# Kernel optimization log

Hardware: AMD Instinct MI355X
Metric: run time of the kernel (lower is better)

The kernel has to match this reference:

```python
import jax, jax.numpy as jnp
import numpy as np

SR = 44100.0
BLK = 512          # block_size (hop)
WL = 2048          # win_length
W4 = WL // 4
B, NF = 4, 512
L = NF * BLK


def _framewise_conv(src, kernels, pad_l, pad_r):
    """Per-(batch,frame) 1D cross-correlation via grouped conv.
    src: (B,F,blk), kernels: (B,F,kw) -> (B,F,blk+pad_l+pad_r-kw+1)."""
    b, f, blk = src.shape
    kw = kernels.shape[-1]
    s = jnp.pad(src, ((0, 0), (0, 0), (pad_l, pad_r))).reshape(1, b * f, blk + pad_l + pad_r)
    k = kernels.reshape(b * f, 1, kw)
    out = jax.lax.conv_general_dilated(
        s, k, window_strides=(1,), padding='VALID',
        feature_group_count=b * f, dimension_numbers=('NCH', 'OIH', 'NCH'))
    return out.reshape(b, f, -1)


def _overlap_add(frames, hop, out_len):
    """frames: (B,F,FL) -> (B,out_len) overlap-add with stride hop (== F.fold)."""
    b, f, fl = frames.shape
    idx = jnp.arange(f)[:, None] * hop + jnp.arange(fl)[None, :]  # (F,FL)
    out = jnp.zeros((b, out_len), frames.dtype)
    return out.at[:, idx].add(frames)


def setup_inputs() -> dict:
    key = jax.random.key(0)
    k1, k2, k3, k4, k5 = jax.random.split(key, 5)
    f0_frames = jax.random.uniform(k1, (B, NF, 1), jnp.float32) * 320.0 + 80.0  # 80-400 Hz
    hk = jax.random.normal(k2, (B, NF, WL), jnp.float32) * (1.0 / np.sqrt(WL))
    hks = jax.random.normal(k3, (B, NF, W4), jnp.float32) * (1.0 / np.sqrt(W4))
    nk = jax.random.normal(k4, (B, NF, W4), jnp.float32) * (1.0 / np.sqrt(W4))
    static_noise = jax.random.uniform(k5, (WL * 127,), jnp.float32) * 2.0 - 1.0
    return {"f0_frames": f0_frames, "harmonic_filt_kernel": hk,
            "harmonic_filt_kernel_short": hks, "noise_filt_kernel": nk,
            "static_noise": static_noise}


def reference(f0_frames, harmonic_filt_kernel, harmonic_filt_kernel_short,
              noise_filt_kernel, static_noise):
    b, nf, _ = f0_frames.shape
    # f0 upsampled to sample rate: (B, L)
    f0 = jnp.repeat(f0_frames, BLK, axis=2).reshape(b, -1)
    # phase accumulator, fractional part (f0 > 0 so frac == mod 1)
    x = jnp.mod(jnp.cumsum(f0 / SR, axis=1), 1.0)
    pix = jnp.pi * x
    a = jnp.round(SR / jnp.clip(f0, 20.0, None) * 0.5) * 2.0 + 1.0
    # band-limited impulse-train-like harmonic source (Dirichlet kernel)
    harmonic_source = jnp.where(pix < 1e-8, 1.0,
                                jnp.sin(a * pix) / (a * jnp.sin(pix)))
    harmonic_source = harmonic_source.reshape(b, nf, BLK)
    # tiled static noise, same for all batch items
    reps = L // static_noise.shape[0] + 1
    noise = jnp.tile(static_noise * 0.3162, reps)[:L].reshape(1, nf, BLK)
    noise = jnp.broadcast_to(noise, (b, nf, BLK))
    # short per-frame FIR on harmonic source and noise (kernel len WL//4)
    hs_short = _framewise_conv(harmonic_source, harmonic_filt_kernel_short, W4, W4 - 1)
    nz = _framewise_conv(noise, noise_filt_kernel, W4, W4 - 1)
    # overlap-add mix, crop to L samples
    mix = _overlap_add(nz + hs_short, BLK, L + W4)[:, :L]
    # long per-frame FIR (kernel len WL) on the mixed signal
    src2 = mix.reshape(b, nf, BLK)
    h2 = _framewise_conv(src2, harmonic_filt_kernel, WL, WL - 1)
    out = _overlap_add(h2, BLK, L + WL)[:, :L]
    return jnp.clip(out, -1.0, 1.0)
```

## Files before the change

### kernel.cpp

```cpp
#include <hip/hip_runtime.h>


#define BLKS  512
#define WL    2048
#define W4    512
#define NB    4
#define NFR   512
#define LTOT  (NFR*BLKS)
#define NCH   (LTOT/16)
#define SN_LEN 260096

typedef float f4 __attribute__((ext_vector_type(4)));

static __device__ __forceinline__ void step16(const f4 hA, const f4 hB, const f4 x,
                                              float& a0, float& a1, float& a2, float& a3) {
    a0 += hB.x*x.x; a0 += hB.y*x.y; a0 += hB.z*x.z; a0 += hB.w*x.w;
    a1 += hA.w*x.x; a1 += hB.x*x.y; a1 += hB.y*x.z; a1 += hB.z*x.w;
    a2 += hA.z*x.x; a2 += hA.w*x.y; a2 += hB.x*x.z; a2 += hB.y*x.w;
    a3 += hA.y*x.x; a3 += hA.z*x.y; a3 += hA.w*x.z; a3 += hB.x*x.w;
}

static __device__ __forceinline__ void seg4(const float* __restrict__ P, int c0,
                                            const float* __restrict__ S,
                                            float& a0, float& a1, float& a2, float& a3) {
    f4 hA = *(const f4*)(P + c0 - 4);
    #pragma unroll 4
    for (int m0 = 0; m0 < 512; m0 += 4) {
        f4 hB = *(const f4*)(P + c0 + m0);
        f4 x  = *(const f4*)(S + m0);
        step16(hA, hB, x, a0, a1, a2, a3);
        hA = hB;
    }
}

static __device__ __forceinline__ void seg4x2(const float* __restrict__ Ph,
                                              const float* __restrict__ Pn, int c0,
                                              const float* __restrict__ Sh,
                                              const float* __restrict__ Sn,
                                              float& a0, float& a1, float& a2, float& a3) {
    f4 hA = *(const f4*)(Ph + c0 - 4);
    f4 nA = *(const f4*)(Pn + c0 - 4);
    #pragma unroll 2
    for (int m0 = 0; m0 < 512; m0 += 4) {
        f4 hB = *(const f4*)(Ph + c0 + m0);
        f4 nB = *(const f4*)(Pn + c0 + m0);
        f4 xh = *(const f4*)(Sh + m0);
        f4 xn = *(const f4*)(Sn + m0);
        a0 += hB.x*xh.x + nB.x*xn.x;  a0 += hB.y*xh.y + nB.y*xn.y;
        a0 += hB.z*xh.z + nB.z*xn.z;  a0 += hB.w*xh.w + nB.w*xn.w;
        a1 += hA.w*xh.x + nA.w*xn.x;  a1 += hB.x*xh.y + nB.x*xn.y;
        a1 += hB.y*xh.z + nB.y*xn.z;  a1 += hB.z*xh.w + nB.z*xn.w;
        a2 += hA.z*xh.x + nA.z*xn.x;  a2 += hA.w*xh.y + nA.w*xn.y;
        a2 += hB.x*xh.z + nB.x*xn.z;  a2 += hB.y*xh.w + nB.y*xn.w;
        a3 += hA.y*xh.x + nA.y*xn.x;  a3 += hA.z*xh.y + nA.z*xn.y;
        a3 += hA.w*xh.z + nA.w*xn.z;  a3 += hB.x*xh.w + nB.x*xn.w;
        hA = hB; nA = nB;
    }
}

__global__ void __launch_bounds__(256) k_scan_a(const float* __restrict__ f0_frames,
                                                float* __restrict__ L0,
                                                float* __restrict__ L1) {
    int b = blockIdx.y;
    int chunk = blockIdx.x * 256 + threadIdx.x;
    int g0 = chunk * 16;
    float d = f0_frames[b*NFR + (g0 >> 9)] / 44100.0f;
    float* o = L0 + (size_t)b*LTOT + g0;
    float acc = 0.0f;
    #pragma unroll
    for (int j = 0; j < 16; ++j) { acc = acc + d; o[j] = acc; }
    L1[(size_t)b*NCH + chunk] = acc;
}

__global__ void __launch_bounds__(1024) k_scan_b(float* __restrict__ L1g) {
    __shared__ float sL2[1024];
    __shared__ float sL3[64];
    __shared__ float sL4[4];
    int b = blockIdx.x, tid = threadIdx.x;
    float* L1 = L1g + (size_t)b*NCH;
    {
        float* p = L1 + tid*16;
        float acc = 0.0f;
        #pragma unroll
        for (int j = 0; j < 16; ++j) { acc = acc + p[j]; p[j] = acc; }
        sL2[tid] = acc;
    }
    __syncthreads();
    if (tid < 64) {
        float acc = 0.0f;
        #pragma unroll
        for (int j = 0; j < 16; ++j) { acc = acc + sL2[tid*16+j]; sL2[tid*16+j] = acc; }
        sL3[tid] = acc;
    }
    __syncthreads();
    if (tid < 4) {
        float acc = 0.0f;
        #pragma unroll
        for (int j = 0; j < 16; ++j) { acc = acc + sL3[tid*16+j]; sL3[tid*16+j] = acc; }
        sL4[tid] = acc;
    }
    __syncthreads();
    if (tid == 0) {
        float acc = 0.0f;
        #pragma unroll
        for (int j = 0; j < 4; ++j) { acc = acc + sL4[j]; sL4[j] = acc; }
    }
    __syncthreads();
    if (tid >= 16 && tid < 64) sL3[tid] = sL3[tid] + sL4[tid/16 - 1];
    __syncthreads();
    if (tid >= 16) sL2[tid] = sL2[tid] + sL3[tid/16 - 1];
    __syncthreads();
    for (int i = tid; i < NCH; i += 1024)
        if (i >= 16) L1[i] = L1[i] + sL2[i/16 - 1];
}

__global__ void __launch_bounds__(256) k_source(const float* __restrict__ f0_frames,
                                                const float* __restrict__ L0,
                                                const float* __restrict__ L1,
                                                float* __restrict__ hs) {
    int F = blockIdx.x, b = blockIdx.y;
    int tid = threadIdx.x;
    float f0 = f0_frames[b*NFR + F];
    float af = rintf(44100.0f / fmaxf(f0, 20.0f) * 0.5f) * 2.0f + 1.0f;
    const float PIF = 3.14159274101257324f;
    for (int i = tid; i < BLKS; i += 256) {
        int g = F*BLKS + i;
        float c = L0[(size_t)b*LTOT + g];
        if (g >= 16) c = c + L1[(size_t)b*NCH + (g >> 4) - 1];
        float x = c - floorf(c);
        float pix = PIF * x;
        float v;
        if (pix < 1e-8f) v = 1.0f;
        else             v = sinf(af * pix) / (af * sinf(pix));
        hs[(size_t)b*LTOT + g] = v;
    }
}

__global__ void __launch_bounds__(128) k_mix(const float* __restrict__ hs,
                                             const float* __restrict__ sn,
                                             const float* __restrict__ hks,
                                             const float* __restrict__ nk,
                                             float* __restrict__ mixg) {
    __shared__ float sH[1024], sN[1024];
    __shared__ float Hh1[1024], Hn1[1024];
    __shared__ float Hh0[1024], Hn0[1024];
    int F = blockIdx.x, b = blockIdx.y, tid = threadIdx.x;
    int s0 = (F - 1) * BLKS;
    for (int i = tid; i < 1024; i += 128) {
        int s = s0 + i;
        float hv = 0.0f, nv = 0.0f;
        if (s >= 0) { hv = hs[(size_t)b*LTOT + s]; nv = sn[s % SN_LEN] * 0.3162f; }
        sH[i] = hv; sN[i] = nv;
    }
    const float* kh = hks + ((size_t)b*NFR + F)*W4;
    const float* kn = nk  + ((size_t)b*NFR + F)*W4;
    for (int i = tid; i < 1024; i += 128) {
        Hh1[i] = (i < 512) ? kh[i] : 0.0f;
        Hn1[i] = (i < 512) ? kn[i] : 0.0f;
        float hp = 0.0f, np_ = 0.0f;
        if (i >= 512 && F >= 1) { hp = kh[i - 1024]; np_ = kn[i - 1024]; }
        Hh0[i] = hp; Hn0[i] = np_;
    }
    __syncthreads();
    int j0 = tid * 4;
    float a0=0.f, a1=0.f, a2=0.f, a3=0.f;
    seg4x2(Hh1, Hn1, 512 - j0, sH + 512, sN + 512, a0, a1, a2, a3);
    seg4x2(Hh0 + 512, Hn0 + 512, -j0, sH, sN, a0, a1, a2, a3);
    f4 r; r.x=a0; r.y=a1; r.z=a2; r.w=a3;
    *(f4*)(mixg + (size_t)b*LTOT + F*BLKS + j0) = r;
}

__global__ void __launch_bounds__(128) k_out(const float* __restrict__ mixg,
                                             const float* __restrict__ hk,
                                             float* __restrict__ outp) {
    __shared__ float sM[2560];
    __shared__ float H4[1024];
    __shared__ float H0[1024];
    int F = blockIdx.x, b = blockIdx.y, tid = threadIdx.x;
    int s0 = (F - 4) * BLKS;
    const float* mb = mixg + (size_t)b*LTOT;
    for (int i = tid; i < 2560; i += 128) {
        int s = s0 + i;
        sM[i] = (s >= 0) ? mb[s] : 0.0f;
    }
    const float* rF = hk + ((size_t)b*NFR + F)*WL;
    for (int i = tid; i < 1024; i += 128)
        H4[i] = (i < 512) ? rF[1536 + i] : 0.0f;
    for (int i = tid; i < 1024; i += 128) {
        float v = 0.0f;
        if (i >= 512 && F >= 4) v = hk[((size_t)b*NFR + F - 4)*WL + (i - 512)];
        H0[i] = v;
    }
    __syncthreads();
    int j0 = tid * 4;
    float a0=0.f, a1=0.f, a2=0.f, a3=0.f;
    #pragma unroll 1
    for (int q = 1; q <= 3; ++q) {
        int fs = F - 4 + q;
        if (fs < 0) continue;
        const float* P = hk + ((size_t)b*NFR + fs)*WL;
        seg4(P, 512*q - j0, sM + 512*q, a0, a1, a2, a3);
    }
    seg4(H4, 512 - j0, sM + 2048, a0, a1, a2, a3);
    seg4(H0 + 512, -j0, sM, a0, a1, a2, a3);
    f4 r;
    r.x = fminf(fmaxf(a0, -1.0f), 1.0f);
    r.y = fminf(fmaxf(a1, -1.0f), 1.0f);
    r.z = fminf(fmaxf(a2, -1.0f), 1.0f);
    r.w = fminf(fmaxf(a3, -1.0f), 1.0f);
    *(f4*)(outp + (size_t)b*LTOT + F*BLKS + j0) = r;
}

extern "C" void kernel_launch(void* const* d_in, const int* in_sizes, int n_in,
                              void* d_out, int out_size, void* d_ws, size_t ws_size,
                              hipStream_t stream) {
    const float* f0  = (const float*)d_in[0];
    const float* hk  = (const float*)d_in[1];
    const float* hks = (const float*)d_in[2];
    const float* nk  = (const float*)d_in[3];
    const float* sn  = (const float*)d_in[4];
    float* outp = (float*)d_out;

    float* ws   = (float*)d_ws;
    float* L0   = ws;
    float* L1   = L0 + (size_t)NB*LTOT;
    float* hsb  = L1 + (size_t)NB*NCH;
    float* mixg = hsb + (size_t)NB*LTOT;

    hipLaunchKernelGGL(k_scan_a, dim3(64, NB),  dim3(256),  0, stream, f0, L0, L1);
    hipLaunchKernelGGL(k_scan_b, dim3(NB),      dim3(1024), 0, stream, L1);
    hipLaunchKernelGGL(k_source, dim3(NFR, NB), dim3(256),  0, stream, f0, L0, L1, hsb);
    hipLaunchKernelGGL(k_mix,    dim3(NFR, NB), dim3(128),  0, stream, hsb, sn, hks, nk, mixg);
    hipLaunchKernelGGL(k_out,    dim3(NFR, NB), dim3(128),  0, stream, mixg, hk, outp);
}
```

Measured before the change: 209.3 us.

## Swap roles: stage filter kernels in LDS, stream signal from global, 8 outputs/thread

The mix and output FIR kernels now keep the per-frame filter taps in shared memory and read the signal segments straight from global memory, instead of staging the signal and reading the taps globally. Each thread now computes 8 consecutive outputs rather than 4, and blocks shrink to 64 threads, so each loaded value is reused across more outputs. The noise scaling moves into the inner loop. This aims to cut redundant loads and raise arithmetic intensity. In exchange it uses more registers per thread and fewer threads per block, which may reduce latency hiding.

After: 176.6 us. -15.6%, faster.

```diff
diff --git a/kernel.cpp b/kernel.cpp
--- a/kernel.cpp
+++ b/kernel.cpp
@@ -12,49 +12,62 @@
 
 typedef float f4 __attribute__((ext_vector_type(4)));
 
-static __device__ __forceinline__ void step16(const f4 hA, const f4 hB, const f4 x,
-                                              float& a0, float& a1, float& a2, float& a3) {
-    a0 += hB.x*x.x; a0 += hB.y*x.y; a0 += hB.z*x.z; a0 += hB.w*x.w;
-    a1 += hA.w*x.x; a1 += hB.x*x.y; a1 += hB.y*x.z; a1 += hB.z*x.w;
-    a2 += hA.z*x.x; a2 += hA.w*x.y; a2 += hB.x*x.z; a2 += hB.y*x.w;
-    a3 += hA.y*x.x; a3 += hA.z*x.y; a3 += hA.w*x.z; a3 += hB.x*x.w;
-}
-
-static __device__ __forceinline__ void seg4(const float* __restrict__ P, int c0,
+#define ROW1(r, W0,W1,W2,W3) \
+    a##r += W0*x.x; a##r += W1*x.y; a##r += W2*x.z; a##r += W3*x.w;
+
+static __device__ __forceinline__ void seg8(const float* __restrict__ P, int c0,
                                             const float* __restrict__ S,
-                                            float& a0, float& a1, float& a2, float& a3) {
-    f4 hA = *(const f4*)(P + c0 - 4);
+                                            float&a0,float&a1,float&a2,float&a3,
+                                            float&a4,float&a5,float&a6,float&a7) {
+    f4 A = *(const f4*)(P + c0 - 8);
+    f4 B = *(const f4*)(P + c0 - 4);
     #pragma unroll 4
     for (int m0 = 0; m0 < 512; m0 += 4) {
-        f4 hB = *(const f4*)(P + c0 + m0);
-        f4 x  = *(const f4*)(S + m0);
-        step16(hA, hB, x, a0, a1, a2, a3);
-        hA = hB;
-    }
-}
-
-static __device__ __forceinline__ void seg4x2(const float* __restrict__ Ph,
+        f4 C = *(const f4*)(P + c0 + m0);
+        f4 x = *(const f4*)(S + m0);
+        ROW1(0, C.x,C.y,C.z,C.w)
+        ROW1(1, B.w,C.x,C.y,C.z)
+        ROW1(2, B.z,B.w,C.x,C.y)
+        ROW1(3, B.y,B.z,B.w,C.x)
+        ROW1(4, B.x,B.y,B.z,B.w)
+        ROW1(5, A.w,B.x,B.y,B.z)
+        ROW1(6, A.z,A.w,B.x,B.y)
+        ROW1(7, A.y,A.z,A.w,B.x)
+        A = B; B = C;
+    }
+}
+
+#define ROW2(r, H0,H1,H2,H3, N0,N1,N2,N3) \
+    a##r += H0*xh.x; a##r += N0*xn.x;  a##r += H1*xh.y; a##r += N1*xn.y; \
+    a##r += H2*xh.z; a##r += N2*xn.z;  a##r += H3*xh.w; a##r += N3*xn.w;
+
+static __device__ __forceinline__ void segmix(const float* __restrict__ Ph,
                                               const float* __restrict__ Pn, int c0,
                                               const float* __restrict__ Sh,
                                               const float* __restrict__ Sn,
-                                              float& a0, float& a1, float& a2, float& a3) {
-    f4 hA = *(const f4*)(Ph + c0 - 4);
-    f4 nA = *(const f4*)(Pn + c0 - 4);
+                                              float&a0,float&a1,float&a2,float&a3,
+                                              float&a4,float&a5,float&a6,float&a7) {
+    f4 Ah = *(const f4*)(Ph + c0 - 8);
+    f4 Bh = *(const f4*)(Ph + c0 - 4);
+    f4 An = *(const f4*)(Pn + c0 - 8);
+    f4 Bn = *(const f4*)(Pn + c0 - 4);
     #pragma unroll 2
     for (int m0 = 0; m0 < 512; m0 += 4) {
-        f4 hB = *(const f4*)(Ph + c0 + m0);
-        f4 nB = *(const f4*)(Pn + c0 + m0);
+        f4 Ch = *(const f4*)(Ph + c0 + m0);
+        f4 Cn = *(const f4*)(Pn + c0 + m0);
         f4 xh = *(const f4*)(Sh + m0);
-        f4 xn = *(const f4*)(Sn + m0);
-        a0 += hB.x*xh.x + nB.x*xn.x;  a0 += hB.y*xh.y + nB.y*xn.y;
-        a0 += hB.z*xh.z + nB.z*xn.z;  a0 += hB.w*xh.w + nB.w*xn.w;
-        a1 += hA.w*xh.x + nA.w*xn.x;  a1 += hB.x*xh.y + nB.x*xn.y;
-        a1 += hB.y*xh.z + nB.y*xn.z;  a1 += hB.z*xh.w + nB.z*xn.w;
-        a2 += hA.z*xh.x + nA.z*xn.x;  a2 += hA.w*xh.y + nA.w*xn.y;
-        a2 += hB.x*xh.z + nB.x*xn.z;  a2 += hB.y*xh.w + nB.y*xn.w;
-        a3 += hA.y*xh.x + nA.y*xn.x;  a3 += hA.z*xh.y + nA.z*xn.y;
-        a3 += hA.w*xh.z + nA.w*xn.z;  a3 += hB.x*xh.w + nB.x*xn.w;
-        hA = hB; nA = nB;
+        f4 xr = *(const f4*)(Sn + m0);
+        f4 xn; xn.x = xr.x*0.3162f; xn.y = xr.y*0.3162f;
+               xn.z = xr.z*0.3162f; xn.w = xr.w*0.3162f;
+        ROW2(0, Ch.x,Ch.y,Ch.z,Ch.w, Cn.x,Cn.y,Cn.z,Cn.w)
+        ROW2(1, Bh.w,Ch.x,Ch.y,Ch.z, Bn.w,Cn.x,Cn.y,Cn.z)
+        ROW2(2, Bh.z,Bh.w,Ch.x,Ch.y, Bn.z,Bn.w,Cn.x,Cn.y)
+        ROW2(3, Bh.y,Bh.z,Bh.w,Ch.x, Bn.y,Bn.z,Bn.w,Cn.x)
+        ROW2(4, Bh.x,Bh.y,Bh.z,Bh.w, Bn.x,Bn.y,Bn.z,Bn.w)
+        ROW2(5, Ah.w,Bh.x,Bh.y,Bh.z, An.w,Bn.x,Bn.y,Bn.z)
+        ROW2(6, Ah.z,Ah.w,Bh.x,Bh.y, An.z,An.w,Bn.x,Bn.y)
+        ROW2(7, Ah.y,Ah.z,Ah.w,Bh.x, An.y,An.z,An.w,Bn.x)
+        Ah = Bh; Bh = Ch; An = Bn; Bn = Cn;
     }
 }
 
@@ -136,79 +149,82 @@
     }
 }
 
-__global__ void __launch_bounds__(128) k_mix(const float* __restrict__ hs,
-                                             const float* __restrict__ sn,
-                                             const float* __restrict__ hks,
-                                             const float* __restrict__ nk,
-                                             float* __restrict__ mixg) {
-    __shared__ float sH[1024], sN[1024];
-    __shared__ float Hh1[1024], Hn1[1024];
-    __shared__ float Hh0[1024], Hn0[1024];
+__global__ void __launch_bounds__(64) k_mix(const float* __restrict__ hs,
+                                            const float* __restrict__ sn,
+                                            const float* __restrict__ hks,
+                                            const float* __restrict__ nk,
+                                            float* __restrict__ mixg) {
+    __shared__ float Wh1[1024], Wn1[1024], Wh0[1024], Wn0[1024];
     int F = blockIdx.x, b = blockIdx.y, tid = threadIdx.x;
-    int s0 = (F - 1) * BLKS;
-    for (int i = tid; i < 1024; i += 128) {
-        int s = s0 + i;
-        float hv = 0.0f, nv = 0.0f;
-        if (s >= 0) { hv = hs[(size_t)b*LTOT + s]; nv = sn[s % SN_LEN] * 0.3162f; }
-        sH[i] = hv; sN[i] = nv;
-    }
-    const float* kh = hks + ((size_t)b*NFR + F)*W4;
-    const float* kn = nk  + ((size_t)b*NFR + F)*W4;
-    for (int i = tid; i < 1024; i += 128) {
-        Hh1[i] = (i < 512) ? kh[i] : 0.0f;
-        Hn1[i] = (i < 512) ? kn[i] : 0.0f;
-        float hp = 0.0f, np_ = 0.0f;
-        if (i >= 512 && F >= 1) { hp = kh[i - 1024]; np_ = kn[i - 1024]; }
-        Hh0[i] = hp; Hn0[i] = np_;
-    }
-    __syncthreads();
-    int j0 = tid * 4;
-    float a0=0.f, a1=0.f, a2=0.f, a3=0.f;
-    seg4x2(Hh1, Hn1, 512 - j0, sH + 512, sN + 512, a0, a1, a2, a3);
-    seg4x2(Hh0 + 512, Hn0 + 512, -j0, sH, sN, a0, a1, a2, a3);
-    f4 r; r.x=a0; r.y=a1; r.z=a2; r.w=a3;
-    *(f4*)(mixg + (size_t)b*LTOT + F*BLKS + j0) = r;
-}
-
-__global__ void __launch_bounds__(128) k_out(const float* __restrict__ mixg,
-                                             const float* __restrict__ hk,
-                                             float* __restrict__ outp) {
-    __shared__ float sM[2560];
-    __shared__ float H4[1024];
-    __shared__ float H0[1024];
+    const f4* khF4 = (const f4*)(hks + ((size_t)b*NFR + F)*W4);
+    const f4* knF4 = (const f4*)(nk  + ((size_t)b*NFR + F)*W4);
+    f4 z; z.x = z.y = z.z = z.w = 0.0f;
+    for (int i = tid; i < 256; i += 64) {
+        ((f4*)Wh1)[i] = (i < 128) ? khF4[i] : z;
+        ((f4*)Wn1)[i] = (i < 128) ? knF4[i] : z;
+        ((f4*)Wh0)[i] = (i >= 128 && F >= 1) ? khF4[i - 256] : z;
+        ((f4*)Wn0)[i] = (i >= 128 && F >= 1) ? knF4[i - 256] : z;
+    }
+    __syncthreads();
+    int j0 = tid * 8;
+    float a0=0,a1=0,a2=0,a3=0,a4=0,a5=0,a6=0,a7=0;
+    const float* hsF = hs + (size_t)b*LTOT + (size_t)F*BLKS;
+    segmix(Wh1, Wn1, 512 - j0, hsF, sn + (F*BLKS) % SN_LEN,
+           a0,a1,a2,a3,a4,a5,a6,a7);
+    if (F >= 1)
+        segmix(Wh0, Wn0, 512 - j0, hsF - BLKS, sn + ((F-1)*BLKS) % SN_LEN,
+               a0,a1,a2,a3,a4,a5,a6,a7);
+    float* o = mixg + (size_t)b*LTOT + (size_t)F*BLKS + j0;
+    f4 r0; r0.x=a0; r0.y=a1; r0.z=a2; r0.w=a3;
+    f4 r1; r1.x=a4; r1.y=a5; r1.z=a6; r1.w=a7;
+    *(f4*)o = r0; *(f4*)(o + 4) = r1;
+}
+
+__global__ void __launch_bounds__(64) k_out(const float* __restrict__ mixg,
+                                            const float* __restrict__ hk,
+                                            float* __restrict__ outp) {
+    __shared__ float Wc[5][1024];
     int F = blockIdx.x, b = blockIdx.y, tid = threadIdx.x;
-    int s0 = (F - 4) * BLKS;
+    f4 z; z.x = z.y = z.z = z.w = 0.0f;
+    #pragma unroll
+    for (int q = 0; q < 5; ++q) {
+        int fs = F - 4 + q;
+        const f4* row4 = (const f4*)(hk + ((size_t)b*NFR + fs)*WL);
+        f4* Wp = (f4*)Wc[q];
+        for (int i = tid; i < 256; i += 64) {
+            f4 v = z;
+            if (fs >= 0) {
+                if (q == 0)      { if (i >= 128) v = row4[i - 128]; }
+                else if (q == 4) { if (i < 128)  v = row4[384 + i]; }
+                else             v = row4[128*(q-1) + i];
+            }
+            Wp[i] = v;
+        }
+    }
+    __syncthreads();
+    int j0 = tid * 8;
+    float a0=0,a1=0,a2=0,a3=0,a4=0,a5=0,a6=0,a7=0;
     const float* mb = mixg + (size_t)b*LTOT;
-    for (int i = tid; i < 2560; i += 128) {
-        int s = s0 + i;
-        sM[i] = (s >= 0) ? mb[s] : 0.0f;
-    }
-    const float* rF = hk + ((size_t)b*NFR + F)*WL;
-    for (int i = tid; i < 1024; i += 128)
-        H4[i] = (i < 512) ? rF[1536 + i] : 0.0f;
-    for (int i = tid; i < 1024; i += 128) {
-        float v = 0.0f;
-        if (i >= 512 && F >= 4) v = hk[((size_t)b*NFR + F - 4)*WL + (i - 512)];
-        H0[i] = v;
-    }
-    __syncthreads();
-    int j0 = tid * 4;
-    float a0=0.f, a1=0.f, a2=0.f, a3=0.f;
     #pragma unroll 1
     for (int q = 1; q <= 3; ++q) {
         int fs = F - 4 + q;
         if (fs < 0) continue;
-        const float* P = hk + ((size_t)b*NFR + fs)*WL;
-        seg4(P, 512*q - j0, sM + 512*q, a0, a1, a2, a3);
-    }
-    seg4(H4, 512 - j0, sM + 2048, a0, a1, a2, a3);
-    seg4(H0 + 512, -j0, sM, a0, a1, a2, a3);
-    f4 r;
-    r.x = fminf(fmaxf(a0, -1.0f), 1.0f);
-    r.y = fminf(fmaxf(a1, -1.0f), 1.0f);
-    r.z = fminf(fmaxf(a2, -1.0f), 1.0f);
-    r.w = fminf(fmaxf(a3, -1.0f), 1.0f);
-    *(f4*)(outp + (size_t)b*LTOT + F*BLKS + j0) = r;
+        seg8(Wc[q], 512 - j0, mb + (size_t)fs*BLKS, a0,a1,a2,a3,a4,a5,a6,a7);
+    }
+    seg8(Wc[4], 512 - j0, mb + (size_t)F*BLKS, a0,a1,a2,a3,a4,a5,a6,a7);
+    if (F >= 4)
+        seg8(Wc[0], 512 - j0, mb + (size_t)(F-4)*BLKS, a0,a1,a2,a3,a4,a5,a6,a7);
+    float* o = outp + (size_t)b*LTOT + (size_t)F*BLKS + j0;
+    f4 r0, r1;
+    r0.x = fminf(fmaxf(a0, -1.0f), 1.0f);
+    r0.y = fminf(fmaxf(a1, -1.0f), 1.0f);
+    r0.z = fminf(fmaxf(a2, -1.0f), 1.0f);
+    r0.w = fminf(fmaxf(a3, -1.0f), 1.0f);
+    r1.x = fminf(fmaxf(a4, -1.0f), 1.0f);
+    r1.y = fminf(fmaxf(a5, -1.0f), 1.0f);
+    r1.z = fminf(fmaxf(a6, -1.0f), 1.0f);
+    r1.w = fminf(fmaxf(a7, -1.0f), 1.0f);
+    *(f4*)o = r0; *(f4*)(o + 4) = r1;
 }
 
 extern "C" void kernel_launch(void* const* d_in, const int* in_sizes, int n_in,
@@ -230,6 +246,6 @@
     hipLaunchKernelGGL(k_scan_a, dim3(64, NB),  dim3(256),  0, stream, f0, L0, L1);
     hipLaunchKernelGGL(k_scan_b, dim3(NB),      dim3(1024), 0, stream, L1);
     hipLaunchKernelGGL(k_source, dim3(NFR, NB), dim3(256),  0, stream, f0, L0, L1, hsb);
-    hipLaunchKernelGGL(k_mix,    dim3(NFR, NB), dim3(128),  0, stream, hsb, sn, hks, nk, mixg);
-    hipLaunchKernelGGL(k_out,    dim3(NFR, NB), dim3(128),  0, stream, mixg, hk, outp);
-}
+    hipLaunchKernelGGL(k_mix,    dim3(NFR, NB), dim3(64),   0, stream, hsb, sn, hks, nk, mixg);
+    hipLaunchKernelGGL(k_out,    dim3(NFR, NB), dim3(64),   0, stream, mixg, hk, outp);
+}
```
